# Kernel tuning notes

Measured on AMD Instinct MI355X. Metric: run time of the kernel, lower is better.

## Reference

```python
import jax, jax.numpy as jnp
import numpy as np

LEAK = 0.2          # LeakyReLU negative slope
NEG = -9e15         # mask fill value from the original module
N, FIN, FOUT = 8192, 256, 128


def setup_inputs() -> dict:
    key = jax.random.key(0)
    k1, k2, k3, k4 = jax.random.split(key, 4)
    x = jax.random.normal(k1, (N, FIN), dtype=jnp.float32)
    # dense 0/1 adjacency mask, p(edge) ~= 0.5
    adj = jax.random.randint(k2, (N, N), 0, 2, dtype=jnp.int32)
    # xavier_uniform with gain sqrt(2)
    gW = np.sqrt(2.0) * np.sqrt(6.0 / (FIN + FOUT))
    W = jax.random.uniform(k3, (FIN, FOUT), dtype=jnp.float32, minval=-gW, maxval=gW)
    ga = np.sqrt(2.0) * np.sqrt(6.0 / (FOUT + 1))
    a = jax.random.uniform(k4, (FOUT, 1), dtype=jnp.float32, minval=-ga, maxval=ga)
    return {"x": x, "adj": adj, "W": W, "a": a}


def reference(x, adj, W, a):
    # h = X W                                     [N, FOUT]
    h = x @ W
    # alpha_j = a . h_j  -- the original's h.repeat(N,1) @ a reduces to this,
    # since every row block of the repeat is identical.
    alpha = jnp.squeeze(h @ a, axis=-1)           # [N]
    e = jax.nn.leaky_relu(alpha, LEAK)            # [N]
    # e_ij depends only on column j; broadcast across rows, then mask.
    scores = jnp.where(adj > 0, e[None, :], NEG)  # [N, N]
    attention = jax.nn.softmax(scores, axis=1)    # [N, N]
    # dropout: eval mode (training=False) -> identity
    h_prime = attention @ h                       # [N, FOUT]
    return h_prime
```

## Files before the change

### kernel.cpp

```cpp
#include <hip/hip_runtime.h>
#include <hip/hip_bf16.h>

#define NN 8192
#define FIN 256
#define FOUT 128
#define FP 144
#define KSPLIT 4
#define KCH (NN / KSPLIT)
#define NT (KCH / 32)
#define PANEL_BYTES (FP * 256)

typedef __attribute__((ext_vector_type(8))) short short8;
typedef __attribute__((ext_vector_type(4))) float f32x4;
typedef __attribute__((ext_vector_type(4))) int i32x4;
typedef __attribute__((ext_vector_type(4))) unsigned int u32x4;
typedef unsigned short u16;
typedef unsigned int u32;

__device__ inline u16 bf16r(float v) {
  return __builtin_bit_cast(u16, __float2bfloat16(v));
}

__global__ __launch_bounds__(256) void k_prep(const float* __restrict__ x,
                                              const float* __restrict__ W,
                                              const float* __restrict__ a,
                                              u16* __restrict__ gT) {
  __shared__ float xs[32 * 256];
  __shared__ float ap[4][16];
  __shared__ float wsh[32];
  __shared__ u16 gsh[32][132];
  const int t = threadIdx.x;
  const int r0 = blockIdx.x * 32;

  const float4* xg = (const float4*)(x + (size_t)r0 * FIN);
  float4* xs4 = (float4*)xs;
#pragma unroll
  for (int p = 0; p < 8; ++p) xs4[p * 256 + t] = xg[p * 256 + t];
  __syncthreads();

  const int f = t & 127;
  const int half = t >> 7;
  float acc[16];
#pragma unroll
  for (int i = 0; i < 16; ++i) acc[i] = 0.f;

  const float4* xsr = (const float4*)(xs + half * 16 * 256);
  for (int k4 = 0; k4 < 64; ++k4) {
    float w0 = W[(k4 * 4 + 0) * FOUT + f];
    float w1 = W[(k4 * 4 + 1) * FOUT + f];
    float w2 = W[(k4 * 4 + 2) * FOUT + f];
    float w3 = W[(k4 * 4 + 3) * FOUT + f];
#pragma unroll
    for (int i = 0; i < 16; ++i) {
      float4 xv = xsr[i * 64 + k4];
      acc[i] = fmaf(xv.x, w0, acc[i]);
      acc[i] = fmaf(xv.y, w1, acc[i]);
      acc[i] = fmaf(xv.z, w2, acc[i]);
      acc[i] = fmaf(xv.w, w3, acc[i]);
    }
  }

  const float af = a[f];
  float part[16];
#pragma unroll
  for (int i = 0; i < 16; ++i) part[i] = acc[i] * af;
#pragma unroll
  for (int i = 0; i < 16; ++i) {
#pragma unroll
    for (int off = 32; off >= 1; off >>= 1) part[i] += __shfl_xor(part[i], off);
  }
  const int wvid = t >> 6;
  if ((t & 63) == 0) {
#pragma unroll
    for (int i = 0; i < 16; ++i) ap[wvid][i] = part[i];
  }
  __syncthreads();
  if (t < 32) {
    int i = t & 15, hh = t >> 4;
    float alpha = ap[hh * 2][i] + ap[hh * 2 + 1][i];
    float ee = alpha > 0.f ? alpha : 0.2f * alpha;
    float wv = __expf(fminf(ee, 80.f));
    wsh[t] = wv;
  }
  __syncthreads();

#pragma unroll
  for (int i = 0; i < 16; ++i) {
    int row = half * 16 + i;
    gsh[row][f] = bf16r(acc[i] * wsh[row]);
  }
  if (t < 240) {
    int fz = 129 + (t >> 4);
    int j = (t & 15) * 2;
    *(u32*)&gT[(size_t)fz * NN + r0 + j] = 0u;
  }
  if (t < 32) gT[(size_t)128 * NN + r0 + t] = bf16r(wsh[t]);
  __syncthreads();

  const int ff = t >> 1;
  const int jc = (t & 1) * 16;
  u16* dst = gT + (size_t)ff * NN + r0 + jc;
#pragma unroll
  for (int q = 0; q < 4; ++q) {
    ushort4 v;
    v.x = gsh[jc + q * 4 + 0][ff];
    v.y = gsh[jc + q * 4 + 1][ff];
    v.z = gsh[jc + q * 4 + 2][ff];
    v.w = gsh[jc + q * 4 + 3][ff];
    *(ushort4*)(dst + q * 4) = v;
  }
}

__global__ __launch_bounds__(256, 2) void k_mm(const int* __restrict__ adj,
                                               const u16* __restrict__ gT,
                                               float* __restrict__ numerP) {
  extern __shared__ char smem[];
  const int t = threadIdx.x;
  const int lane = t & 63;
  const int wv = t >> 6;
  const int i0 = blockIdx.x * 64;
  const int ks = blockIdx.y;
  const int kbase = ks * KCH;
  const int rloc = lane & 15;
  const int ksl = lane >> 4;

  const int* aptr = adj + (size_t)(i0 + wv * 16 + rloc) * NN + kbase + ksl * 8;

  f32x4 acc[9];
#pragma unroll
  for (int n = 0; n < 9; ++n) acc[n] = (f32x4){0.f, 0.f, 0.f, 0.f};

  i32x4 Aa[4], Ab[4];

  auto ISSUE_B = [&](int p, int buf) {
    const char* gTb = (const char*)gT;
#pragma unroll
    for (int i = 0; i < 9; ++i) {
      int gi = wv * 9 + i;
      int fr = gi * 4 + ksl;
      const char* src = gTb + (size_t)fr * (NN * 2) +
                        (size_t)(kbase + p * 128) * 2 +
                        ((rloc * 16) ^ ((fr & 7) << 4));
      char* dst = smem + buf * PANEL_BYTES + gi * 1024;
      __builtin_amdgcn_global_load_lds((const u32*)src, (u32*)dst, 16, 0, 0);
    }
  };

  ISSUE_B(0, 0);
  __builtin_amdgcn_sched_barrier(0);
#pragma unroll
  for (int q = 0; q < 4; ++q) {
    const i32x4* pp = (const i32x4*)(aptr + q * 32);
    Aa[q] = pp[0];
    Ab[q] = pp[1];
  }
  asm volatile("s_waitcnt vmcnt(8)" ::: "memory");
  __builtin_amdgcn_s_barrier();
  __builtin_amdgcn_sched_barrier(0);

#pragma unroll 1
  for (int p = 0; p < 16; ++p) {
    const int buf = p & 1;
    if (p < 15) {
      ISSUE_B(p + 1, buf ^ 1);
      __builtin_amdgcn_sched_barrier(0);
    }
#pragma unroll
    for (int q = 0; q < 4; ++q) {
      const int kt = p * 4 + q;
      i32x4 a0 = Aa[q], a1 = Ab[q];
      if (kt + 4 < NT) {
        const i32x4* pp = (const i32x4*)(aptr + (kt + 4) * 32);
        Aa[q] = pp[0];
        Ab[q] = pp[1];
      }
      u32 p0 = ((u32)a0[0] + ((u32)a0[1] << 16)) * 0x3F80u;
      u32 p1 = ((u32)a0[2] + ((u32)a0[3] << 16)) * 0x3F80u;
      u32 p2 = ((u32)a1[0] + ((u32)a1[1] << 16)) * 0x3F80u;
      u32 p3 = ((u32)a1[2] + ((u32)a1[3] << 16)) * 0x3F80u;
      u32x4 pv = {p0, p1, p2, p3};
      short8 fa = __builtin_bit_cast(short8, pv);
      const char* B = smem + buf * PANEL_BYTES;
      const int X = q * 64 + ksl * 16;
#pragma unroll
      for (int n = 0; n < 9; ++n) {
        int fr = n * 16 + rloc;
        short8 fb = *(const short8*)(B + fr * 256 + (X ^ ((fr & 7) << 4)));
        acc[n] = __builtin_amdgcn_mfma_f32_16x16x32_bf16(fa, fb, acc[n], 0, 0, 0);
      }
    }
    if (p < 15) {
      asm volatile("s_waitcnt vmcnt(8)" ::: "memory");
      __builtin_amdgcn_s_barrier();
      __builtin_amdgcn_sched_barrier(0);
    }
  }

  float* np = numerP + ((size_t)ks * NN + i0 + wv * 16) * FP;
#pragma unroll
  for (int qq = 0; qq < 4; ++qq) {
    int row = ksl * 4 + qq;
#pragma unroll
    for (int n = 0; n < 9; ++n)
      np[(size_t)row * FP + n * 16 + rloc] = acc[n][qq];
  }
}

__global__ __launch_bounds__(256) void k_comb(const float* __restrict__ nP,
                                              float* __restrict__ out) {
  const int idx = blockIdx.x * 256 + threadIdx.x;
  const int row = idx >> 5;
  const int fc = (idx & 31) * 4;
  float4 s = {0.f, 0.f, 0.f, 0.f};
  float d = 0.f;
#pragma unroll
  for (int ks = 0; ks < KSPLIT; ++ks) {
    const float* base = nP + ((size_t)ks * NN + row) * FP;
    float4 nv = *(const float4*)(base + fc);
    s.x += nv.x;
    s.y += nv.y;
    s.z += nv.z;
    s.w += nv.w;
    d += base[128];
  }
  float inv = 1.0f / d;
  float4 o;
  o.x = s.x * inv;
  o.y = s.y * inv;
  o.z = s.z * inv;
  o.w = s.w * inv;
  *(float4*)(out + (size_t)row * FOUT + fc) = o;
}

extern "C" void kernel_launch(void* const* d_in, const int* in_sizes, int n_in,
                              void* d_out, int out_size, void* d_ws, size_t ws_size,
                              hipStream_t stream) {
  const float* x = (const float*)d_in[0];
  const int* adj = (const int*)d_in[1];
  const float* W = (const float*)d_in[2];
  const float* a = (const float*)d_in[3];
  float* out = (float*)d_out;

  char* ws = (char*)d_ws;
  u16* gT = (u16*)(ws + (size_t)1 * 1024 * 1024);
  float* numerP = (float*)(ws + (size_t)8 * 1024 * 1024);

  hipLaunchKernelGGL(k_prep, dim3(NN / 32), dim3(256), 0, stream, x, W, a, gT);
  hipLaunchKernelGGL(k_mm, dim3(NN / 64, KSPLIT), dim3(256), 2 * PANEL_BYTES, stream,
                     adj, gT, numerP);
  hipLaunchKernelGGL(k_comb, dim3((NN * 32) / 256), dim3(256), 0, stream, numerP, out);
}
```

Before: 108.4 us.

## Double rows per wave in adjacency MFMA kernel and double K-split

Each wave now computes two 16-row tiles that share every B fragment read from LDS, so the gT panel loaded per block serves 128 rows instead of 64. The K split is doubled to keep the grid size the same, and the A prefetch is restructured to load the whole next panel per iteration. s_setprio is raised around the MFMA section. The cost is doubled accumulator and A-prefetch registers, which may pressure occupancy at launch bound 2. It also doubles the partial-sum traffic that k_comb has to reduce. Note that k_comb still loops over KSPLIT, so it picks up the new split.

```diff
diff --git a/kernel.cpp b/kernel.cpp
--- a/kernel.cpp
+++ b/kernel.cpp
@@ -5,9 +5,10 @@
 #define FIN 256
 #define FOUT 128
 #define FP 144
-#define KSPLIT 4
+#define KSPLIT 8
 #define KCH (NN / KSPLIT)
 #define NT (KCH / 32)
+#define NP (KCH / 128)
 #define PANEL_BYTES (FP * 256)
 
 typedef __attribute__((ext_vector_type(8))) short short8;
@@ -118,19 +119,23 @@
   const int t = threadIdx.x;
   const int lane = t & 63;
   const int wv = t >> 6;
-  const int i0 = blockIdx.x * 64;
+  const int i0 = blockIdx.x * 128;
   const int ks = blockIdx.y;
   const int kbase = ks * KCH;
   const int rloc = lane & 15;
   const int ksl = lane >> 4;
 
-  const int* aptr = adj + (size_t)(i0 + wv * 16 + rloc) * NN + kbase + ksl * 8;
-
-  f32x4 acc[9];
-#pragma unroll
-  for (int n = 0; n < 9; ++n) acc[n] = (f32x4){0.f, 0.f, 0.f, 0.f};
-
-  i32x4 Aa[4], Ab[4];
+  const int* aptr0 = adj + (size_t)(i0 + wv * 32 + rloc) * NN + kbase + ksl * 8;
+  const int* aptr1 = aptr0 + (size_t)16 * NN;
+
+  f32x4 acc0[9], acc1[9];
+#pragma unroll
+  for (int n = 0; n < 9; ++n) {
+    acc0[n] = (f32x4){0.f, 0.f, 0.f, 0.f};
+    acc1[n] = (f32x4){0.f, 0.f, 0.f, 0.f};
+  }
+
+  i32x4 A0a[4], A0b[4], A1a[4], A1b[4];
 
   auto ISSUE_B = [&](int p, int buf) {
     const char* gTb = (const char*)gT;
@@ -146,63 +151,74 @@
     }
   };
 
+  auto LDA = [&](int q, int kt) {
+    const i32x4* p0 = (const i32x4*)(aptr0 + kt * 32);
+    const i32x4* p1 = (const i32x4*)(aptr1 + kt * 32);
+    A0a[q] = p0[0];
+    A0b[q] = p0[1];
+    A1a[q] = p1[0];
+    A1b[q] = p1[1];
+  };
+
+  auto PACK = [](i32x4 a0, i32x4 a1) {
+    u32 p0 = ((u32)a0[0] + ((u32)a0[1] << 16)) * 0x3F80u;
+    u32 p1 = ((u32)a0[2] + ((u32)a0[3] << 16)) * 0x3F80u;
+    u32 p2 = ((u32)a1[0] + ((u32)a1[1] << 16)) * 0x3F80u;
+    u32 p3 = ((u32)a1[2] + ((u32)a1[3] << 16)) * 0x3F80u;
+    u32x4 pv = {p0, p1, p2, p3};
+    return __builtin_bit_cast(short8, pv);
+  };
+
   ISSUE_B(0, 0);
   __builtin_amdgcn_sched_barrier(0);
 #pragma unroll
-  for (int q = 0; q < 4; ++q) {
-    const i32x4* pp = (const i32x4*)(aptr + q * 32);
-    Aa[q] = pp[0];
-    Ab[q] = pp[1];
-  }
-  asm volatile("s_waitcnt vmcnt(8)" ::: "memory");
+  for (int q = 0; q < 4; ++q) LDA(q, q);
+  asm volatile("s_waitcnt vmcnt(16)" ::: "memory");
   __builtin_amdgcn_s_barrier();
   __builtin_amdgcn_sched_barrier(0);
 
 #pragma unroll 1
-  for (int p = 0; p < 16; ++p) {
+  for (int p = 0; p < NP; ++p) {
     const int buf = p & 1;
-    if (p < 15) {
+    const bool more = (p + 1 < NP);
+    if (more) {
       ISSUE_B(p + 1, buf ^ 1);
       __builtin_amdgcn_sched_barrier(0);
     }
+    __builtin_amdgcn_s_setprio(1);
 #pragma unroll
     for (int q = 0; q < 4; ++q) {
-      const int kt = p * 4 + q;
-      i32x4 a0 = Aa[q], a1 = Ab[q];
-      if (kt + 4 < NT) {
-        const i32x4* pp = (const i32x4*)(aptr + (kt + 4) * 32);
-        Aa[q] = pp[0];
-        Ab[q] = pp[1];
-      }
-      u32 p0 = ((u32)a0[0] + ((u32)a0[1] << 16)) * 0x3F80u;
-      u32 p1 = ((u32)a0[2] + ((u32)a0[3] << 16)) * 0x3F80u;
-      u32 p2 = ((u32)a1[0] + ((u32)a1[1] << 16)) * 0x3F80u;
-      u32 p3 = ((u32)a1[2] + ((u32)a1[3] << 16)) * 0x3F80u;
-      u32x4 pv = {p0, p1, p2, p3};
-      short8 fa = __builtin_bit_cast(short8, pv);
+      short8 fa0 = PACK(A0a[q], A0b[q]);
+      short8 fa1 = PACK(A1a[q], A1b[q]);
+      if (more) LDA(q, (p + 1) * 4 + q);
       const char* B = smem + buf * PANEL_BYTES;
       const int X = q * 64 + ksl * 16;
 #pragma unroll
       for (int n = 0; n < 9; ++n) {
         int fr = n * 16 + rloc;
         short8 fb = *(const short8*)(B + fr * 256 + (X ^ ((fr & 7) << 4)));
-        acc[n] = __builtin_amdgcn_mfma_f32_16x16x32_bf16(fa, fb, acc[n], 0, 0, 0);
+        acc0[n] = __builtin_amdgcn_mfma_f32_16x16x32_bf16(fa0, fb, acc0[n], 0, 0, 0);
+        acc1[n] = __builtin_amdgcn_mfma_f32_16x16x32_bf16(fa1, fb, acc1[n], 0, 0, 0);
       }
     }
-    if (p < 15) {
-      asm volatile("s_waitcnt vmcnt(8)" ::: "memory");
+    __builtin_amdgcn_s_setprio(0);
+    if (more) {
+      asm volatile("s_waitcnt vmcnt(16)" ::: "memory");
       __builtin_amdgcn_s_barrier();
       __builtin_amdgcn_sched_barrier(0);
     }
   }
 
-  float* np = numerP + ((size_t)ks * NN + i0 + wv * 16) * FP;
+  float* np0 = numerP + ((size_t)ks * NN + i0 + wv * 32) * FP;
+  float* np1 = np0 + (size_t)16 * FP;
 #pragma unroll
   for (int qq = 0; qq < 4; ++qq) {
     int row = ksl * 4 + qq;
 #pragma unroll
-    for (int n = 0; n < 9; ++n)
-      np[(size_t)row * FP + n * 16 + rloc] = acc[n][qq];
+    for (int n = 0; n < 9; ++n) {
+      np0[(size_t)row * FP + n * 16 + rloc] = acc0[n][qq];
+      np1[(size_t)row * FP + n * 16 + rloc] = acc1[n][qq];
+    }
   }
 }
 
@@ -246,7 +262,7 @@
   float* numerP = (float*)(ws + (size_t)8 * 1024 * 1024);
 
   hipLaunchKernelGGL(k_prep, dim3(NN / 32), dim3(256), 0, stream, x, W, a, gT);
-  hipLaunchKernelGGL(k_mm, dim3(NN / 64, KSPLIT), dim3(256), 2 * PANEL_BYTES, stream,
+  hipLaunchKernelGGL(k_mm, dim3(NN / 128, KSPLIT), dim3(256), 2 * PANEL_BYTES, stream,
                      adj, gT, numerP);
   hipLaunchKernelGGL(k_comb, dim3((NN * 32) / 256), dim3(256), 0, stream, numerP, out);
 }
```

Result: slower. 130.4 us (+20.3%).
